# Kernel tuning notes

Measured on AMD Instinct MI355X. Metric: run time of the kernel, lower is better.

Reference implementation:

```python
import jax, jax.numpy as jnp
import numpy as np
import math

B, S, E, H, FF = 2, 2048, 768, 12, 3072
D = E // H
SCALING = 1.0
EPS = 1e-5


def layer_norm(x, g, b):
    mu = jnp.mean(x, axis=-1, keepdims=True)
    var = jnp.var(x, axis=-1, keepdims=True)
    return (x - mu) * jax.lax.rsqrt(var + EPS) * g + b


def setup_inputs() -> dict:
    key = jax.random.key(0)
    ks = jax.random.split(key, 16)
    s_e = 1.0 / math.sqrt(E)
    s_f = 1.0 / math.sqrt(FF)
    inp = {
        "x": jax.random.normal(ks[0], (B, S, E), dtype=jnp.float32),
        "Wq": jax.random.uniform(ks[1], (E, E), jnp.float32, -s_e, s_e),
        "bq": jnp.zeros((E,), jnp.float32),
        "Wk": jax.random.uniform(ks[2], (E, E), jnp.float32, -s_e, s_e),
        "bk": jnp.zeros((E,), jnp.float32),
        "Wv": jax.random.uniform(ks[3], (E, E), jnp.float32, -s_e, s_e),
        "bv": jnp.zeros((E,), jnp.float32),
        "Wo": jax.random.uniform(ks[4], (E, E), jnp.float32, -s_e, s_e),
        "bo": jnp.zeros((E,), jnp.float32),
        "W1": jax.random.uniform(ks[5], (E, FF), jnp.float32, -s_e, s_e),
        "b1": jnp.zeros((FF,), jnp.float32),
        "W2": jax.random.uniform(ks[6], (FF, E), jnp.float32, -s_f, s_f),
        "b2": jnp.zeros((E,), jnp.float32),
        "g1": jnp.ones((E,), jnp.float32),
        "be1": jnp.zeros((E,), jnp.float32),
        "g2": jnp.ones((E,), jnp.float32),
        "be2": jnp.zeros((E,), jnp.float32),
    }
    return inp


def reference(x, Wq, bq, Wk, bk, Wv, bv, Wo, bo, W1, b1, W2, b2, g1, be1, g2, be2):
    # --- multi-head attention with ALiBi-style symmetric distance bias ---
    q = (x @ Wq + bq).reshape(B, S, H, D)
    k = (x @ Wk + bk).reshape(B, S, H, D)
    v = (x @ Wv + bv).reshape(B, S, H, D)
    scores = jnp.einsum("bqhd,bkhd->bhqk", q, k) / math.sqrt(D)
    pos = jnp.arange(S)
    alibi = -SCALING * jnp.abs(pos[None, :] - pos[:, None]).astype(jnp.float32)  # [S,S]
    scores = scores + alibi  # broadcast over [B,H]
    attn_map = jax.nn.softmax(scores, axis=-1)  # [B,H,S,S]
    ctx = jnp.einsum("bhqk,bkhd->bqhd", attn_map, v).reshape(B, S, E)
    attn_out = ctx @ Wo + bo
    # --- residual + norm, FFN, residual + norm (dropout = eval/identity) ---
    h = layer_norm(x + attn_out, g1, be1)
    ff = jax.nn.relu(h @ W1 + b1) @ W2 + b2
    out = layer_norm(h + ff, g2, be2)
    return (out, attn_map)
```

## Files before the change

kernel.cpp:

```cpp
#include <hip/hip_runtime.h>
#include <stdint.h>

static constexpr int cB = 2, cS = 2048, cE = 768, cH = 12, cFF = 3072, cD = 64;
static constexpr int cM = cB * cS;

typedef __bf16 bf16x8 __attribute__((ext_vector_type(8)));
typedef float f32x4 __attribute__((ext_vector_type(4)));

__device__ __forceinline__ unsigned short f2bf(float f) {
    union { float f; unsigned int u; } v; v.f = f;
    unsigned int r = v.u + 0x7fffu + ((v.u >> 16) & 1u);
    return (unsigned short)(r >> 16);
}

__device__ __forceinline__ void load_lds16(const unsigned short* g, unsigned short* l) {
    __builtin_amdgcn_global_load_lds(
        (const __attribute__((address_space(1))) unsigned int*)(g),
        (__attribute__((address_space(3))) unsigned int*)(l), 16, 0, 0);
}

template<int BM, int BN, int EPI>
__global__ __launch_bounds__(256) void gemm_nt(
    const unsigned short* __restrict__ Ab,
    const unsigned short* __restrict__ Btp,
    float* __restrict__ outF,
    unsigned short* __restrict__ outB,
    const float* __restrict__ bias0,
    const float* __restrict__ bias1,
    const float* __restrict__ bias2,
    const float* __restrict__ resid,
    int M, int N, int K, long sB)
{
    constexpr int MI = BM / 32, NI = BN / 32;
    __shared__ alignas(16) unsigned short Al[BM * 64];
    __shared__ alignas(16) unsigned short Bl[BN * 64];
    const int tid = threadIdx.x;
    const int lane = tid & 63, wave = tid >> 6;
    const int wm = wave >> 1, wn = wave & 1;
    const int bz = blockIdx.z;
    const int m0 = blockIdx.y * BM, n0 = blockIdx.x * BN;
    const int ln = lane & 15, lg = lane >> 4;
    const int sw = ln & 7;

    const unsigned short* Bt = Btp + (size_t)bz * sB;

    f32x4 acc[MI][NI];
#pragma unroll
    for (int i = 0; i < MI; i++)
#pragma unroll
        for (int j = 0; j < NI; j++) acc[i][j] = (f32x4){0.f, 0.f, 0.f, 0.f};

    for (int k0 = 0; k0 < K; k0 += 64) {
        __syncthreads();
#pragma unroll
        for (int it = 0; it < BM / 32; ++it) {
            int idx = tid + it * 256;
            int r = idx >> 3, c8 = idx & 7;
            int cs = c8 ^ (r & 7);
            load_lds16(Ab + (size_t)(m0 + r) * K + k0 + cs * 8, &Al[idx * 8]);
        }
#pragma unroll
        for (int it = 0; it < BN / 32; ++it) {
            int idx = tid + it * 256;
            int r = idx >> 3, c8 = idx & 7;
            int cs = c8 ^ (r & 7);
            load_lds16(Bt + (size_t)(n0 + r) * K + k0 + cs * 8, &Bl[idx * 8]);
        }
        __syncthreads();
#pragma unroll
        for (int ks = 0; ks < 2; ++ks) {
            bf16x8 av[MI], bv[NI];
#pragma unroll
            for (int i = 0; i < MI; i++) {
                int row = wm * (BM / 2) + 16 * i + ln;
                av[i] = *(const bf16x8*)&Al[row * 64 + ((ks * 4 + lg) ^ sw) * 8];
            }
#pragma unroll
            for (int j = 0; j < NI; j++) {
                int row = wn * (BN / 2) + 16 * j + ln;
                bv[j] = *(const bf16x8*)&Bl[row * 64 + ((ks * 4 + lg) ^ sw) * 8];
            }
#pragma unroll
            for (int i = 0; i < MI; i++)
#pragma unroll
                for (int j = 0; j < NI; j++)
                    acc[i][j] = __builtin_amdgcn_mfma_f32_16x16x32_bf16(av[i], bv[j], acc[i][j], 0, 0, 0);
        }
    }

#pragma unroll
    for (int i = 0; i < MI; i++) {
#pragma unroll
        for (int j = 0; j < NI; j++) {
#pragma unroll
            for (int r = 0; r < 4; r++) {
                int m = m0 + wm * (BM / 2) + 16 * i + lg * 4 + r;
                int n = n0 + wn * (BN / 2) + 16 * j + ln;
                float v = acc[i][j][r];
                if constexpr (EPI == 0) {
                    const float* bia = (bz == 0) ? bias0 : ((bz == 1) ? bias1 : bias2);
                    v += bia[n];
                    int b = m >> 11, s = m & 2047, h = n >> 6, d = n & 63;
                    outB[(size_t)bz * ((size_t)cB * cH * cS * cD) +
                         ((((size_t)b * cH + h) * cS + s) << 6) + d] = f2bf(v);
                } else if constexpr (EPI == 3) {
                    v += bias0[n] + resid[(size_t)m * N + n];
                    outF[(size_t)m * N + n] = v;
                } else {
                    v = fmaxf(v + bias0[n], 0.f);
                    outB[(size_t)m * N + n] = f2bf(v);
                }
            }
        }
    }
}

__global__ __launch_bounds__(256, 3) void attn_fused(
    const unsigned short* __restrict__ Qh,
    const unsigned short* __restrict__ Kh,
    const unsigned short* __restrict__ Vt,
    float* __restrict__ attn,
    unsigned short* __restrict__ ctxb)
{
    constexpr int VS = 136;
    __shared__ alignas(16) unsigned short Kl[128 * 64];
    __shared__ alignas(16) unsigned short Vl[64 * 128];
    __shared__ alignas(16) unsigned short Pb[64 * VS];
    __shared__ float rs2[2][64];
    __shared__ float rsinv[64];

    const int tid = threadIdx.x;
    const int lane = tid & 63, wave = tid >> 6;
    const int wm = wave >> 1, wn = wave & 1;
    const int ln = lane & 15, lg = lane >> 4;
    const int sw = ln & 7;
    const int m0 = blockIdx.x * 64;
    const int bh = blockIdx.y;

    const int nt_lo = max(0, (m0 - 120) / 128);
    const int nt_hi = min(15, (m0 + 183) / 128);

    const unsigned short* Qg = Qh + ((size_t)bh * cS + m0) * cD;
    const unsigned short* Kg = Kh + (size_t)bh * cS * cD;
    const unsigned short* Vg = Vt + (size_t)bh * cD * cS;
    float* attng = attn + (size_t)bh * cS * cS;

#pragma unroll
    for (int it = 0; it < 2; ++it) {
        int idx = tid + it * 256;
        int r = idx >> 3, c8 = idx & 7;
        int cs = c8 ^ (r & 7);
        load_lds16(Qg + r * cD + cs * 8, &Vl[idx * 8]);
    }
    __syncthreads();
    bf16x8 qf[2][2];
#pragma unroll
    for (int ks = 0; ks < 2; ++ks)
#pragma unroll
        for (int i = 0; i < 2; i++)
            qf[ks][i] = *(const bf16x8*)&Vl[(wm * 32 + 16 * i + ln) * 64 + ((ks * 4 + lg) ^ sw) * 8];

    float psum[8];
#pragma unroll
    for (int k = 0; k < 8; k++) psum[k] = 0.f;

    for (int nt = nt_lo; nt <= nt_hi; ++nt) {
        __syncthreads();
#pragma unroll
        for (int it = 0; it < 4; ++it) {
            int idx = tid + it * 256;
            int r = idx >> 3, c8 = idx & 7;
            int cs = c8 ^ (r & 7);
            load_lds16(Kg + (size_t)(nt * 128 + r) * cD + cs * 8, &Kl[idx * 8]);
        }
        __syncthreads();
        f32x4 acc[2][4];
#pragma unroll
        for (int i = 0; i < 2; i++)
#pragma unroll
            for (int j = 0; j < 4; j++) acc[i][j] = (f32x4){0.f, 0.f, 0.f, 0.f};
#pragma unroll
        for (int ks = 0; ks < 2; ++ks) {
            bf16x8 b[4];
#pragma unroll
            for (int j = 0; j < 4; j++)
                b[j] = *(const bf16x8*)&Kl[(wn * 64 + 16 * j + ln) * 64 + ((ks * 4 + lg) ^ sw) * 8];
#pragma unroll
            for (int i = 0; i < 2; i++)
#pragma unroll
                for (int j = 0; j < 4; j++)
                    acc[i][j] = __builtin_amdgcn_mfma_f32_16x16x32_bf16(qf[ks][i], b[j], acc[i][j], 0, 0, 0);
        }
#pragma unroll
        for (int i = 0; i < 2; i++)
#pragma unroll
            for (int j = 0; j < 4; j++)
#pragma unroll
                for (int r = 0; r < 4; r++) {
                    int mg = m0 + wm * 32 + 16 * i + lg * 4 + r;
                    int ng = nt * 128 + wn * 64 + 16 * j + ln;
                    psum[i * 4 + r] += __expf(acc[i][j][r] * 0.125f - fabsf((float)(mg - ng)));
                }
    }
#pragma unroll
    for (int k = 0; k < 8; k++) {
        float v = psum[k];
        v += __shfl_xor(v, 1); v += __shfl_xor(v, 2);
        v += __shfl_xor(v, 4); v += __shfl_xor(v, 8);
        psum[k] = v;
    }
    if (ln == 0) {
#pragma unroll
        for (int i = 0; i < 2; i++)
#pragma unroll
            for (int r = 0; r < 4; r++)
                rs2[wn][wm * 32 + 16 * i + lg * 4 + r] = psum[i * 4 + r];
    }
    __syncthreads();
    if (tid < 64) rsinv[tid] = 1.f / (rs2[0][tid] + rs2[1][tid]);
    __syncthreads();
    float invl[8];
#pragma unroll
    for (int i = 0; i < 2; i++)
#pragma unroll
        for (int r = 0; r < 4; r++)
            invl[i * 4 + r] = rsinv[wm * 32 + 16 * i + lg * 4 + r];

    f32x4 oacc[2][2];
#pragma unroll
    for (int i = 0; i < 2; i++)
#pragma unroll
        for (int j = 0; j < 2; j++) oacc[i][j] = (f32x4){0.f, 0.f, 0.f, 0.f};

    for (int nt = nt_lo; nt <= nt_hi; ++nt) {
        __syncthreads();
#pragma unroll
        for (int it = 0; it < 4; ++it) {
            int idx = tid + it * 256;
            int r = idx >> 3, c8 = idx & 7;
            int cs = c8 ^ (r & 7);
            load_lds16(Kg + (size_t)(nt * 128 + r) * cD + cs * 8, &Kl[idx * 8]);
        }
#pragma unroll
        for (int it = 0; it < 4; ++it) {
            int idx = tid + it * 256;
            int r = idx >> 4, c8 = idx & 15;
            int cs = c8 ^ (r & 7);
            load_lds16(Vg + (size_t)r * cS + nt * 128 + cs * 8, &Vl[idx * 8]);
        }
        __syncthreads();
        f32x4 acc[2][4];
#pragma unroll
        for (int i = 0; i < 2; i++)
#pragma unroll
            for (int j = 0; j < 4; j++) acc[i][j] = (f32x4){0.f, 0.f, 0.f, 0.f};
#pragma unroll
        for (int ks = 0; ks < 2; ++ks) {
            bf16x8 b[4];
#pragma unroll
            for (int j = 0; j < 4; j++)
                b[j] = *(const bf16x8*)&Kl[(wn * 64 + 16 * j + ln) * 64 + ((ks * 4 + lg) ^ sw) * 8];
#pragma unroll
            for (int i = 0; i < 2; i++)
#pragma unroll
                for (int j = 0; j < 4; j++)
                    acc[i][j] = __builtin_amdgcn_mfma_f32_16x16x32_bf16(qf[ks][i], b[j], acc[i][j], 0, 0, 0);
        }
#pragma unroll
        for (int i = 0; i < 2; i++)
#pragma unroll
            for (int j = 0; j < 4; j++)
#pragma unroll
                for (int r = 0; r < 4; r++) {
                    int mloc = wm * 32 + 16 * i + lg * 4 + r;
                    int nloc = wn * 64 + 16 * j + ln;
                    int mg = m0 + mloc, ng = nt * 128 + nloc;
                    float p = __expf(acc[i][j][r] * 0.125f - fabsf((float)(mg - ng))) * invl[i * 4 + r];
                    attng[(size_t)mg * cS + ng] = p;
                    Pb[mloc * VS + nloc] = f2bf(p);
                }
        __syncthreads();
#pragma unroll
        for (int ks = 0; ks < 4; ++ks) {
            bf16x8 pa[2], vb[2];
#pragma unroll
            for (int i = 0; i < 2; i++)
                pa[i] = *(const bf16x8*)&Pb[(wm * 32 + 16 * i + ln) * VS + ks * 32 + lg * 8];
#pragma unroll
            for (int j = 0; j < 2; j++) {
                int row = wn * 32 + 16 * j + ln;
                vb[j] = *(const bf16x8*)&Vl[row * 128 + ((ks * 4 + lg) ^ sw) * 8];
            }
#pragma unroll
            for (int i = 0; i < 2; i++)
#pragma unroll
                for (int j = 0; j < 2; j++)
                    oacc[i][j] = __builtin_amdgcn_mfma_f32_16x16x32_bf16(pa[i], vb[j], oacc[i][j], 0, 0, 0);
        }
    }
    {
        int b = bh / cH, h = bh % cH;
#pragma unroll
        for (int i = 0; i < 2; i++)
#pragma unroll
            for (int j = 0; j < 2; j++)
#pragma unroll
                for (int r = 0; r < 4; r++) {
                    int mg = m0 + wm * 32 + 16 * i + lg * 4 + r;
                    int d = wn * 32 + 16 * j + ln;
                    ctxb[((size_t)b * cS + mg) * cE + h * 64 + d] = f2bf(oacc[i][j][r]);
                }
    }
    {
        const f32x4 z4 = {0.f, 0.f, 0.f, 0.f};
        const int c4lo = nt_lo * 32;
        const int c4hi = (nt_hi + 1) * 32;
        for (int r = wave; r < 64; r += 4) {
            f32x4* rowp = (f32x4*)(attng + (size_t)(m0 + r) * cS);
            for (int c = lane; c < c4lo; c += 64) rowp[c] = z4;
            for (int c = c4hi + lane; c < 512; c += 64) rowp[c] = z4;
        }
    }
}

template<bool WH>
__global__ __launch_bounds__(256) void layernorm_k(const float* __restrict__ in,
    const float* __restrict__ g, const float* __restrict__ be,
    float* __restrict__ outF, unsigned short* __restrict__ outB)
{
    const size_t row = blockIdx.x;
    const float* p = in + row * cE;
    const int tid = threadIdx.x;
    float x0 = p[tid], x1 = p[tid + 256], x2 = p[tid + 512];
    float sum = x0 + x1 + x2, sq = x0 * x0 + x1 * x1 + x2 * x2;
    __shared__ float s1[4], s2[4];
    for (int o = 32; o; o >>= 1) { sum += __shfl_xor(sum, o); sq += __shfl_xor(sq, o); }
    if ((tid & 63) == 0) { s1[tid >> 6] = sum; s2[tid >> 6] = sq; }
    __syncthreads();
    sum = s1[0] + s1[1] + s1[2] + s1[3];
    sq  = s2[0] + s2[1] + s2[2] + s2[3];
    float mu = sum * (1.f / cE);
    float var = sq * (1.f / cE) - mu * mu;
    float rstd = rsqrtf(var + 1e-5f);
#pragma unroll
    for (int i = 0; i < 3; i++) {
        int c = tid + 256 * i;
        float xv = (i == 0) ? x0 : ((i == 1) ? x1 : x2);
        float y = (xv - mu) * rstd * g[c] + be[c];
        outF[row * cE + c] = y;
        if constexpr (WH) outB[row * cE + c] = f2bf(y);
    }
}

__global__ __launch_bounds__(256) void prep_all(
    const float* __restrict__ x, unsigned short* __restrict__ xb,
    const float* __restrict__ Wq, const float* __restrict__ Wk,
    const float* __restrict__ Wv, const float* __restrict__ Wo,
    const float* __restrict__ W1, const float* __restrict__ W2,
    unsigned short* __restrict__ Wqt, unsigned short* __restrict__ W1t,
    unsigned short* __restrict__ W2t)
{
    __shared__ float t[32][33];
    int bid = blockIdx.x;
    if (bid < 3072) {
        int i = bid * 256 + threadIdx.x;
        float4 v = ((const float4*)x)[i];
        ushort4 o;
        o.x = f2bf(v.x); o.y = f2bf(v.y); o.z = f2bf(v.z); o.w = f2bf(v.w);
        ((ushort4*)xb)[i] = o;
        return;
    }
    bid -= 3072;
    const float* src; unsigned short* dst; int R, C, tx, ty;
    if (bid < 2304) {
        int m = bid / 576, tt = bid - m * 576;
        src = (m == 0) ? Wq : (m == 1) ? Wk : (m == 2) ? Wv : Wo;
        dst = Wqt + (size_t)m * 589824;
        R = 768; C = 768; tx = tt % 24; ty = tt / 24;
    } else if (bid < 4608) {
        int tt = bid - 2304;
        src = W1; dst = W1t; R = 768; C = 3072; tx = tt % 96; ty = tt / 96;
    } else {
        int tt = bid - 4608;
        src = W2; dst = W2t; R = 3072; C = 768; tx = tt % 24; ty = tt / 24;
    }
    int c0 = tx * 32, r0 = ty * 32;
    int lx = threadIdx.x & 31, ly = threadIdx.x >> 5;
#pragma unroll
    for (int i = 0; i < 32; i += 8) t[ly + i][lx] = src[(size_t)(r0 + ly + i) * C + c0 + lx];
    __syncthreads();
#pragma unroll
    for (int i = 0; i < 32; i += 8) dst[(size_t)(c0 + ly + i) * R + r0 + lx] = f2bf(t[lx][ly + i]);
}

__global__ __launch_bounds__(256) void transpose_bf16_b(const unsigned short* __restrict__ src,
    unsigned short* __restrict__ dst, int R, int C)
{
    __shared__ unsigned short t[32][33];
    int c0 = blockIdx.x * 32, r0 = blockIdx.y * 32;
    size_t zo = (size_t)blockIdx.z * R * C;
    int tx = threadIdx.x & 31, ty = threadIdx.x >> 5;
#pragma unroll
    for (int i = 0; i < 32; i += 8) t[ty + i][tx] = src[zo + (size_t)(r0 + ty + i) * C + c0 + tx];
    __syncthreads();
#pragma unroll
    for (int i = 0; i < 32; i += 8) dst[zo + (size_t)(c0 + ty + i) * R + r0 + tx] = t[tx][ty + i];
}

extern "C" void kernel_launch(void* const* d_in, const int* in_sizes, int n_in,
                              void* d_out, int out_size, void* d_ws, size_t ws_size,
                              hipStream_t stream)
{
    const float* x   = (const float*)d_in[0];
    const float* Wq  = (const float*)d_in[1];
    const float* bq  = (const float*)d_in[2];
    const float* Wk  = (const float*)d_in[3];
    const float* bk  = (const float*)d_in[4];
    const float* Wv  = (const float*)d_in[5];
    const float* bv  = (const float*)d_in[6];
    const float* Wo  = (const float*)d_in[7];
    const float* bo  = (const float*)d_in[8];
    const float* W1  = (const float*)d_in[9];
    const float* b1  = (const float*)d_in[10];
    const float* W2  = (const float*)d_in[11];
    const float* b2  = (const float*)d_in[12];
    const float* g1  = (const float*)d_in[13];
    const float* be1 = (const float*)d_in[14];
    const float* g2  = (const float*)d_in[15];
    const float* be2 = (const float*)d_in[16];

    float* out  = (float*)d_out;
    float* attn = out + (size_t)cB * cS * cE;

    char* ws = (char*)d_ws;
    unsigned short* xb   = (unsigned short*)(ws + 0);
    unsigned short* ctxb = xb;
    unsigned short* Wqt  = (unsigned short*)(ws + 6291456);
    unsigned short* W1t  = (unsigned short*)(ws + 11010048);
    unsigned short* W2t  = (unsigned short*)(ws + 15728640);
    unsigned short* Qh   = (unsigned short*)(ws + 20447232);
    unsigned short* Kh   = (unsigned short*)(ws + 26738688);
    unsigned short* Vh   = (unsigned short*)(ws + 33030144);
    unsigned short* Vt   = (unsigned short*)(ws + 39321600);
    unsigned short* ff1b = Qh;
    float* res1 = (float*)(ws + 45613056);
    float* res2 = res1;
    float* hf   = (float*)(ws + 58195968);
    unsigned short* hb = (unsigned short*)(ws + 70778880);

    prep_all<<<9984, 256, 0, stream>>>(x, xb, Wq, Wk, Wv, Wo, W1, W2, Wqt, W1t, W2t);
    gemm_nt<128, 96, 0><<<dim3(8, 32, 3), 256, 0, stream>>>(
        xb, Wqt, nullptr, Qh, bq, bk, bv, nullptr, cM, cE, cE, 589824);
    transpose_bf16_b<<<dim3(2, 64, cB * cH), 256, 0, stream>>>(Vh, Vt, cS, cD);
    attn_fused<<<dim3(cS / 64, cB * cH), 256, 0, stream>>>(Qh, Kh, Vt, attn, ctxb);
    gemm_nt<128, 96, 3><<<dim3(8, 32, 1), 256, 0, stream>>>(
        ctxb, Wqt + 3 * 589824, res1, nullptr, bo, nullptr, nullptr, x, cM, cE, cE, 0);
    layernorm_k<true><<<cM, 256, 0, stream>>>(res1, g1, be1, hf, hb);
    gemm_nt<128, 128, 4><<<dim3(24, 32, 1), 256, 0, stream>>>(
        hb, W1t, nullptr, ff1b, b1, nullptr, nullptr, nullptr, cM, cFF, cE, 0);
    gemm_nt<128, 96, 3><<<dim3(8, 32, 1), 256, 0, stream>>>(
        ff1b, W2t, res2, nullptr, b2, nullptr, nullptr, hf, cM, cE, cFF, 0);
    layernorm_k<false><<<cM, 256, 0, stream>>>(res2, g2, be2, out, nullptr);
}
```

Measured before the change: 651.2 us.

## Fuse V transpose into QKV GEMM epilogue via LDS staging

The QKV projection GEMM now writes V directly in the transposed per-head layout. It stages the bias-added bf16 tile in shared memory and emits vectorized 16-byte stores, which removes the separate transpose kernel and its extra global round trip. Launch bounds now request 4 blocks per CU. The FFN1 GEMM tile changes from 128x128 to 128x96 with a wider grid. The extra LDS staging and tighter register budget could add spills or sync cost in the epilogue.

Measured after the change: 632.8 us. -2.8%, faster.

```diff
diff --git a/kernel.cpp b/kernel.cpp
--- a/kernel.cpp
+++ b/kernel.cpp
@@ -20,11 +20,12 @@
 }
 
 template<int BM, int BN, int EPI>
-__global__ __launch_bounds__(256) void gemm_nt(
+__global__ __launch_bounds__(256, 4) void gemm_nt(
     const unsigned short* __restrict__ Ab,
     const unsigned short* __restrict__ Btp,
     float* __restrict__ outF,
     unsigned short* __restrict__ outB,
+    unsigned short* __restrict__ outB2,
     const float* __restrict__ bias0,
     const float* __restrict__ bias1,
     const float* __restrict__ bias2,
@@ -32,8 +33,9 @@
     int M, int N, int K, long sB)
 {
     constexpr int MI = BM / 32, NI = BN / 32;
-    __shared__ alignas(16) unsigned short Al[BM * 64];
-    __shared__ alignas(16) unsigned short Bl[BN * 64];
+    __shared__ alignas(16) unsigned short Sh[BM * 64 + BN * 64];
+    unsigned short* Al = Sh;
+    unsigned short* Bl = Sh + BM * 64;
     const int tid = threadIdx.x;
     const int lane = tid & 63, wave = tid >> 6;
     const int wm = wave >> 1, wn = wave & 1;
@@ -88,27 +90,64 @@
         }
     }
 
-#pragma unroll
-    for (int i = 0; i < MI; i++) {
-#pragma unroll
-        for (int j = 0; j < NI; j++) {
-#pragma unroll
-            for (int r = 0; r < 4; r++) {
-                int m = m0 + wm * (BM / 2) + 16 * i + lg * 4 + r;
-                int n = n0 + wn * (BN / 2) + 16 * j + ln;
-                float v = acc[i][j][r];
-                if constexpr (EPI == 0) {
-                    const float* bia = (bz == 0) ? bias0 : ((bz == 1) ? bias1 : bias2);
-                    v += bia[n];
-                    int b = m >> 11, s = m & 2047, h = n >> 6, d = n & 63;
-                    outB[(size_t)bz * ((size_t)cB * cH * cS * cD) +
-                         ((((size_t)b * cH + h) * cS + s) << 6) + d] = f2bf(v);
-                } else if constexpr (EPI == 3) {
-                    v += bias0[n] + resid[(size_t)m * N + n];
-                    outF[(size_t)m * N + n] = v;
-                } else {
-                    v = fmaxf(v + bias0[n], 0.f);
-                    outB[(size_t)m * N + n] = f2bf(v);
+    if constexpr (EPI == 0) {
+        if (bz < 2) {
+            const float* bia = (bz == 0) ? bias0 : bias1;
+#pragma unroll
+            for (int i = 0; i < MI; i++)
+#pragma unroll
+                for (int j = 0; j < NI; j++)
+#pragma unroll
+                    for (int r = 0; r < 4; r++) {
+                        int m = m0 + wm * (BM / 2) + 16 * i + lg * 4 + r;
+                        int n = n0 + wn * (BN / 2) + 16 * j + ln;
+                        float v = acc[i][j][r] + bia[n];
+                        int b = m >> 11, s = m & 2047, h = n >> 6, d = n & 63;
+                        outB[(size_t)bz * ((size_t)cB * cH * cS * cD) +
+                             ((((size_t)b * cH + h) * cS + s) << 6) + d] = f2bf(v);
+                    }
+        } else {
+            constexpr int TS = BM + 8;
+            __syncthreads();
+#pragma unroll
+            for (int i = 0; i < MI; i++)
+#pragma unroll
+                for (int j = 0; j < NI; j++)
+#pragma unroll
+                    for (int r = 0; r < 4; r++) {
+                        int ml = wm * (BM / 2) + 16 * i + lg * 4 + r;
+                        int nl = wn * (BN / 2) + 16 * j + ln;
+                        Sh[nl * TS + ml] = f2bf(acc[i][j][r] + bias2[n0 + nl]);
+                    }
+            __syncthreads();
+            const int b = m0 >> 11, sbase = m0 & 2047;
+#pragma unroll
+            for (int it = 0; it < (BN * BM / 8) / 256; ++it) {
+                int idx = tid + it * 256;
+                int rr = idx >> 4, c8 = idx & 15;
+                uint4 val = *(const uint4*)&Sh[rr * TS + c8 * 8];
+                int ng = n0 + rr;
+                int h = ng >> 6, d = ng & 63;
+                *(uint4*)&outB2[((((size_t)b * cH + h) << 6) + d) * (size_t)cS + sbase + c8 * 8] = val;
+            }
+        }
+    } else {
+#pragma unroll
+        for (int i = 0; i < MI; i++) {
+#pragma unroll
+            for (int j = 0; j < NI; j++) {
+#pragma unroll
+                for (int r = 0; r < 4; r++) {
+                    int m = m0 + wm * (BM / 2) + 16 * i + lg * 4 + r;
+                    int n = n0 + wn * (BN / 2) + 16 * j + ln;
+                    float v = acc[i][j][r];
+                    if constexpr (EPI == 3) {
+                        v += bias0[n] + resid[(size_t)m * N + n];
+                        outF[(size_t)m * N + n] = v;
+                    } else {
+                        v = fmaxf(v + bias0[n], 0.f);
+                        outB[(size_t)m * N + n] = f2bf(v);
+                    }
                 }
             }
         }
@@ -391,20 +430,6 @@
     __syncthreads();
 #pragma unroll
     for (int i = 0; i < 32; i += 8) dst[(size_t)(c0 + ly + i) * R + r0 + lx] = f2bf(t[lx][ly + i]);
-}
-
-__global__ __launch_bounds__(256) void transpose_bf16_b(const unsigned short* __restrict__ src,
-    unsigned short* __restrict__ dst, int R, int C)
-{
-    __shared__ unsigned short t[32][33];
-    int c0 = blockIdx.x * 32, r0 = blockIdx.y * 32;
-    size_t zo = (size_t)blockIdx.z * R * C;
-    int tx = threadIdx.x & 31, ty = threadIdx.x >> 5;
-#pragma unroll
-    for (int i = 0; i < 32; i += 8) t[ty + i][tx] = src[zo + (size_t)(r0 + ty + i) * C + c0 + tx];
-    __syncthreads();
-#pragma unroll
-    for (int i = 0; i < 32; i += 8) dst[zo + (size_t)(c0 + ty + i) * R + r0 + tx] = t[tx][ty + i];
 }
 
 extern "C" void kernel_launch(void* const* d_in, const int* in_sizes, int n_in,
@@ -440,8 +465,7 @@
     unsigned short* W2t  = (unsigned short*)(ws + 15728640);
     unsigned short* Qh   = (unsigned short*)(ws + 20447232);
     unsigned short* Kh   = (unsigned short*)(ws + 26738688);
-    unsigned short* Vh   = (unsigned short*)(ws + 33030144);
-    unsigned short* Vt   = (unsigned short*)(ws + 39321600);
+    unsigned short* Vt   = (unsigned short*)(ws + 33030144);
     unsigned short* ff1b = Qh;
     float* res1 = (float*)(ws + 45613056);
     float* res2 = res1;
@@ -450,15 +474,14 @@
 
     prep_all<<<9984, 256, 0, stream>>>(x, xb, Wq, Wk, Wv, Wo, W1, W2, Wqt, W1t, W2t);
     gemm_nt<128, 96, 0><<<dim3(8, 32, 3), 256, 0, stream>>>(
-        xb, Wqt, nullptr, Qh, bq, bk, bv, nullptr, cM, cE, cE, 589824);
-    transpose_bf16_b<<<dim3(2, 64, cB * cH), 256, 0, stream>>>(Vh, Vt, cS, cD);
+        xb, Wqt, nullptr, Qh, Vt, bq, bk, bv, nullptr, cM, cE, cE, 589824);
     attn_fused<<<dim3(cS / 64, cB * cH), 256, 0, stream>>>(Qh, Kh, Vt, attn, ctxb);
     gemm_nt<128, 96, 3><<<dim3(8, 32, 1), 256, 0, stream>>>(
-        ctxb, Wqt + 3 * 589824, res1, nullptr, bo, nullptr, nullptr, x, cM, cE, cE, 0);
+        ctxb, Wqt + 3 * 589824, res1, nullptr, nullptr, bo, nullptr, nullptr, x, cM, cE, cE, 0);
     layernorm_k<true><<<cM, 256, 0, stream>>>(res1, g1, be1, hf, hb);
-    gemm_nt<128, 128, 4><<<dim3(24, 32, 1), 256, 0, stream>>>(
-        hb, W1t, nullptr, ff1b, b1, nullptr, nullptr, nullptr, cM, cFF, cE, 0);
+    gemm_nt<128, 96, 4><<<dim3(32, 32, 1), 256, 0, stream>>>(
+        hb, W1t, nullptr, ff1b, nullptr, b1, nullptr, nullptr, nullptr, cM, cFF, cE, 0);
     gemm_nt<128, 96, 3><<<dim3(8, 32, 1), 256, 0, stream>>>(
-        ff1b, W2t, res2, nullptr, b2, nullptr, nullptr, hf, cM, cE, cFF, 0);
+        ff1b, W2t, res2, nullptr, nullptr, b2, nullptr, nullptr, hf, cM, cE, cFF, 0);
     layernorm_k<false><<<cM, 256, 0, stream>>>(res2, g2, be2, out, nullptr);
 }
```
